# Kernel optimization log

Measured on AMD Instinct MI355X. Metric: run time of the kernel, lower is better.

The kernel has to match this reference:

```python
import math
import jax, jax.numpy as jnp
import numpy as np

jax.config.update("jax_enable_x64", True)

P_PRIME = 1000003            # prime modulus; p-1 = 2*3*166667
N_FACTORS = (2, 3, 166667)   # prime factors of p-1 (for primitive-root search)
B, NPATCH, L, K, DIM = 4, 784, 9, 16, 28  # batch, patches/sample, patch len, kernels, map dim


def _modpow(base, exp, p, nbits=21):
    """Vectorized modular exponentiation (square-and-multiply), int64, exponents < 2^nbits."""
    shape = jnp.broadcast_shapes(jnp.shape(base), jnp.shape(exp))
    b0 = jnp.broadcast_to(jnp.asarray(base, jnp.int64) % p, shape)
    e = jnp.broadcast_to(jnp.asarray(exp, jnp.int64), shape)
    def body(i, c):
        res, b = c
        res = jnp.where(((e >> i) & 1) == 1, (res * b) % p, res)
        return (res, (b * b) % p)
    res, _ = jax.lax.fori_loop(0, nbits, body, (jnp.ones(shape, jnp.int64), b0))
    return res


def _decrypt_ips(ct0, cts, y, sk_y, g, p):
    """IPFE decrypt + BSGS discrete log. ct0:[B,P] cts:[B,P,L] y:[K,L] sk_y:[K] -> signed ip [K,B,P]."""
    n = p - 1
    powed = _modpow(cts[None], jnp.mod(y, n)[:, None, None, :], p)   # [K,B,P,L]
    num = powed[..., 0]
    for i in range(1, L):                                            # fixed small L=9
        num = (num * powed[..., i]) % p
    denom = _modpow(ct0[None], jnp.mod(sk_y, n)[:, None, None], p)   # [K,B,P]
    val = (num * _modpow(denom, p - 2, p)) % p                       # = g^{<x,y>} mod p (Fermat inverse)
    # baby-step giant-step over group order n
    m = math.isqrt(n - 1) + 1
    n_giant = -(-n // m)
    baby = _modpow(jnp.int64(g), jnp.arange(m, dtype=jnp.int64), p)  # g^j, j in [0,m)
    order = jnp.argsort(baby)
    sb = baby[order]
    ginv_m = _modpow(jnp.int64(g), jnp.int64((n - m) % n), p)        # g^{-m}
    pt = _modpow(ginv_m, jnp.arange(n_giant, dtype=jnp.int64), p)    # g^{-m*i}
    gamma = (val.reshape(-1)[:, None] * pt[None, :]) % p             # [T, n_giant] giant steps
    pos = jnp.clip(jnp.searchsorted(sb, gamma), 0, m - 1)
    hit = sb[pos] == gamma
    cand = jnp.arange(n_giant, dtype=jnp.int64)[None, :] * m + order[pos]
    ip = jnp.min(jnp.where(hit, cand, n), axis=1)                    # unique match: ip = i*m + j
    ip = jnp.where(ip > n // 2, ip - n, ip)                          # signed representative
    return ip.reshape(K, ct0.shape[0], ct0.shape[1])


def _bn(x, g_, b_, m_, v_):
    s = g_ * jax.lax.rsqrt(v_ + 1e-5)
    return (x - m_[None, :, None, None]) * s[None, :, None, None] + b_[None, :, None, None]


def _conv(x, w, b):
    o = jax.lax.conv_general_dilated(x, w, (1, 1), ((1, 1), (1, 1)),
                                     dimension_numbers=("NCHW", "OIHW", "NCHW"))
    return o + b[None, :, None, None]


def _pool(x):
    return jax.lax.reduce_window(x, jnp.array(-jnp.inf, x.dtype), jax.lax.max,
                                 (1, 1, 2, 2), (1, 1, 2, 2), "VALID")


def _forward(ct0, cts, y, sk_y, bias1, bn1_g, bn1_b, bn1_m, bn1_v,
             conv2_w, conv2_b, bn2_g, bn2_b, bn2_m, bn2_v,
             conv3_w, conv3_b, bn3_g, bn3_b, bn3_m, bn3_v,
             fc1_w, fc1_b, fc2_w, fc2_b, g, p):
    ip = _decrypt_ips(ct0, cts, y, sk_y, g, p)                       # [K,B,P] int64
    maps = ip.astype(jnp.float32) / 10000.0 + bias1[:, None, None]   # dequantize + conv1 bias
    feat = jnp.transpose(maps, (1, 0, 2)).reshape(-1, K, DIM, DIM)   # [B,16,28,28]
    feat = _pool(jax.nn.relu(_bn(feat, bn1_g, bn1_b, bn1_m, bn1_v)))
    feat = _pool(jax.nn.relu(_bn(_conv(feat, conv2_w, conv2_b), bn2_g, bn2_b, bn2_m, bn2_v)))
    feat = _pool(jax.nn.relu(_bn(_conv(feat, conv3_w, conv3_b), bn3_g, bn3_b, bn3_m, bn3_v)))
    flat = feat.reshape(feat.shape[0], -1)                           # [B,576]
    h = jax.nn.relu(flat @ fc1_w.T + fc1_b)                          # dropout = identity (eval mode)
    return h @ fc2_w.T + fc2_b                                       # [B,10]


def setup_inputs():
    rng = np.random.default_rng(0)
    p, n = P_PRIME, P_PRIME - 1
    assert all(p % d for d in range(2, math.isqrt(p) + 1))           # p prime
    g = next(gg for gg in range(2, 200)
             if all(pow(gg, n // q, p) != 1 for q in N_FACTORS))      # primitive root mod p
    s = rng.integers(1, n, size=L)                                    # master secret
    pk = [pow(g, int(si), p) for si in s]
    y = rng.integers(-50, 51, size=(K, L)).astype(np.int64)          # round(w*10000)
    x = rng.integers(0, 21, size=(B, NPATCH, L))                     # quantized patch values
    r = rng.integers(1, n, size=(B, NPATCH))
    gx = [pow(g, t, p) for t in range(21)]
    ct0 = np.zeros((B, NPATCH), dtype=np.int64)
    cts = np.zeros((B, NPATCH, L), dtype=np.int64)
    for b in range(B):
        for j in range(NPATCH):
            rr = int(r[b, j])
            ct0[b, j] = pow(g, rr, p)
            for i in range(L):
                cts[b, j, i] = pow(pk[i], rr, p) * gx[x[b, j, i]] % p
    sk_y = np.array([sum(int(s[i]) * int(y[k, i]) for i in range(L)) % n
                     for k in range(K)], dtype=np.int64)
    f32 = lambda a: jnp.asarray(a, jnp.float32)
    def rn(*sh):
        return f32(rng.standard_normal(sh) * 0.1)
    def bnp(c):
        return (f32(1.0 + 0.1 * rng.standard_normal(c)), rn(c), rn(c), f32(rng.random(c) + 0.5))
    bn1_g, bn1_b, bn1_m, bn1_v = bnp(16)
    bn2_g, bn2_b, bn2_m, bn2_v = bnp(32)
    bn3_g, bn3_b, bn3_m, bn3_v = bnp(64)
    return dict(ct0=jnp.asarray(ct0), cts=jnp.asarray(cts),
                y=jnp.asarray(y), sk_y=jnp.asarray(sk_y), bias1=rn(K),
                bn1_g=bn1_g, bn1_b=bn1_b, bn1_m=bn1_m, bn1_v=bn1_v,
                conv2_w=rn(32, 16, 3, 3), conv2_b=rn(32),
                bn2_g=bn2_g, bn2_b=bn2_b, bn2_m=bn2_m, bn2_v=bn2_v,
                conv3_w=rn(64, 32, 3, 3), conv3_b=rn(64),
                bn3_g=bn3_g, bn3_b=bn3_b, bn3_m=bn3_m, bn3_v=bn3_v,
                fc1_w=rn(128, 576), fc1_b=rn(128),
                fc2_w=rn(10, 128), fc2_b=rn(10), g=g, p=p)


def reference(ct0, cts, y, sk_y, bias1, bn1_g, bn1_b, bn1_m, bn1_v,
              conv2_w, conv2_b, bn2_g, bn2_b, bn2_m, bn2_v,
              conv3_w, conv3_b, bn3_g, bn3_b, bn3_m, bn3_v,
              fc1_w, fc1_b, fc2_w, fc2_b, g, p):
    return _forward(ct0, cts, y, sk_y, bias1, bn1_g, bn1_b, bn1_m, bn1_v,
                    conv2_w, conv2_b, bn2_g, bn2_b, bn2_m, bn2_v,
                    conv3_w, conv3_b, bn3_g, bn3_b, bn3_m, bn3_v,
                    fc1_w, fc1_b, fc2_w, fc2_b, g, p)
```

## Files before the change

kernel.cpp:

```cpp
#include <hip/hip_runtime.h>
#include <stdint.h>

#define PRIME 1000003u
#define NORD  1000002u
#define KCH   16
#define BATCH 4
#define NPATCH 784
#define LLEN  9
#define IPMAX 9000
#define NDEC  (KCH*BATCH*NPATCH)
#define MBABY 512
#define NGIANT 36
#define HSLOTS 2048
#define HEMPTY 0xFFFFFFFFu

__device__ __forceinline__ uint32_t mmul(uint32_t a, uint32_t b) {
    uint64_t t = (uint64_t)a * (uint64_t)b;
    uint32_t q = (uint32_t)((t * 2199016ull) >> 41);
    uint32_t r = (uint32_t)t - q * PRIME;
    return (r >= PRIME) ? r - PRIME : r;
}

__device__ __forceinline__ uint32_t mpow(uint32_t base, uint32_t exp) {
    uint32_t r = 1u, b = base;
    while (exp) {
        if (exp & 1u) r = mmul(r, b);
        b = mmul(b, b);
        exp >>= 1;
    }
    return r;
}

__global__ void __launch_bounds__(256) decrypt_dlog(
    const int* __restrict__ ct0, const int* __restrict__ cts,
    const int* __restrict__ y, const int* __restrict__ sk_y,
    const float* __restrict__ bias1,
    const float* __restrict__ bn1_g, const float* __restrict__ bn1_b,
    const float* __restrict__ bn1_m, const float* __restrict__ bn1_v,
    const int* __restrict__ g_in, float* __restrict__ featr) {
    const int tid = threadIdx.x;
    __shared__ uint32_t hash[HSLOTS];

    const uint32_t g = (uint32_t)g_in[0];

    for (int i = tid; i < HSLOTS; i += 256) hash[i] = HEMPTY;
    __syncthreads();
    for (int r = tid; r < MBABY; r += 256) {
        uint32_t key = mpow(g, (uint32_t)r);
        uint32_t h = (key * 0x9E3779B1u) >> 21;
        uint32_t packed = (key << 9) | (uint32_t)r;
        while (atomicCAS(&hash[h], HEMPTY, packed) != HEMPTY)
            h = (h + 1) & (HSLOTS - 1);
    }
    __syncthreads();

    const int gtid = blockIdx.x * 256 + tid;
    if (gtid >= NDEC) return;
    int k = gtid / (BATCH * NPATCH);
    int r = gtid % (BATCH * NPATCH);
    int b = r / NPATCH;
    int j = r % NPATCH;

    const int* crow = cts + ((b * NPATCH) + j) * LLEN;
    const int* yrow = y + k * LLEN;

    uint32_t num_p = 1u, num_n = 1u;
#pragma unroll
    for (int i = 0; i < LLEN; i++) {
        int yi = yrow[i];
        uint32_t c = (uint32_t)crow[i];
        if (yi > 0)       num_p = mmul(num_p, mpow(c, (uint32_t)yi));
        else if (yi < 0)  num_n = mmul(num_n, mpow(c, (uint32_t)(-yi)));
    }
    uint32_t den = mpow((uint32_t)ct0[b * NPATCH + j], (uint32_t)sk_y[k]);
    den = mmul(den, num_n);
    uint32_t val = mmul(num_p, mpow(den, PRIME - 2u));

    uint32_t cur = mmul(val, mpow(g, IPMAX));
    const uint32_t gim = mpow(g, NORD - MBABY);
    int e = 0;
    bool found = false;
    for (int q = 0; q < NGIANT; q++) {
        if (!found) {
            uint32_t hh = (cur * 0x9E3779B1u) >> 21;
            uint32_t v;
            while ((v = hash[hh]) != HEMPTY) {
                if ((v >> 9) == cur) { e = q * MBABY + (int)(v & 511u); found = true; break; }
                hh = (hh + 1) & (HSLOTS - 1);
            }
        }
        cur = mmul(cur, gim);
    }
    int ip = e - IPMAX;

    float sc = bn1_g[k] * rsqrtf(bn1_v[k] + 1e-5f);
    float shf = (bias1[k] - bn1_m[k]) * sc + bn1_b[k];
    float v_ = fmaf((float)ip, sc * 1e-4f, shf);
    featr[((b * KCH) + k) * NPATCH + j] = fmaxf(v_, 0.0f);
}

__global__ void __launch_bounds__(256) conv2_k(
    const float* __restrict__ featr,
    const float* __restrict__ conv2_w, const float* __restrict__ conv2_b,
    const float* __restrict__ bn2_g, const float* __restrict__ bn2_b,
    const float* __restrict__ bn2_m, const float* __restrict__ bn2_v,
    float* __restrict__ s2g) {
    const int b  = blockIdx.x >> 5;
    const int oc = blockIdx.x & 31;
    const int tid = threadIdx.x;

    __shared__ float s1p[16][16][16];
    __shared__ float w[16 * 9];
    __shared__ float co[196];

    for (int i = tid; i < 16 * 16 * 16; i += 256)
        ((float*)s1p)[i] = 0.0f;
    if (tid < 144) w[tid] = conv2_w[oc * 144 + tid];
    __syncthreads();
    for (int i = tid; i < 16 * 196; i += 256) {
        int ic = i / 196, pos = i % 196;
        int yy = pos / 14, xx = pos % 14;
        const float* fp = featr + ((b * 16 + ic) * 784) + (2 * yy) * 28 + 2 * xx;
        s1p[ic][yy + 1][xx + 1] = fmaxf(fmaxf(fp[0], fp[1]), fmaxf(fp[28], fp[29]));
    }
    __syncthreads();

    if (tid < 196) {
        int oh = tid / 14, ow = tid % 14;
        float a0 = 0.0f, a1 = 0.0f, a2 = 0.0f;
#pragma unroll
        for (int ic = 0; ic < 16; ic++) {
            const float* wp = &w[ic * 9];
            const float* sp = &s1p[ic][oh][ow];
            a0 = fmaf(sp[0],  wp[0], fmaf(sp[1],  wp[1], fmaf(sp[2],  wp[2], a0)));
            a1 = fmaf(sp[16], wp[3], fmaf(sp[17], wp[4], fmaf(sp[18], wp[5], a1)));
            a2 = fmaf(sp[32], wp[6], fmaf(sp[33], wp[7], fmaf(sp[34], wp[8], a2)));
        }
        float sc = bn2_g[oc] * rsqrtf(bn2_v[oc] + 1e-5f);
        float shf = bn2_b[oc] - bn2_m[oc] * sc;
        co[tid] = fmaxf((a0 + a1 + a2 + conv2_b[oc]) * sc + shf, 0.0f);
    }
    __syncthreads();

    if (tid < 49) {
        int oh = tid / 7, ow = tid % 7;
        const float* c0 = &co[(2 * oh) * 14 + 2 * ow];
        s2g[((b * 32 + oc) * 49) + tid] =
            fmaxf(fmaxf(c0[0], c0[1]), fmaxf(c0[14], c0[15]));
    }
}

__global__ void __launch_bounds__(64) conv3_k(
    const float* __restrict__ s2g,
    const float* __restrict__ conv3_w, const float* __restrict__ conv3_b,
    const float* __restrict__ bn3_g, const float* __restrict__ bn3_b,
    const float* __restrict__ bn3_m, const float* __restrict__ bn3_v,
    float* __restrict__ s3g) {
    const int b  = blockIdx.x >> 6;
    const int oc = blockIdx.x & 63;
    const int tid = threadIdx.x;

    __shared__ float s2p[32][9][9];
    __shared__ float w[32 * 9];
    __shared__ float co[49];

    for (int i = tid; i < 32 * 81; i += 64)
        ((float*)s2p)[i] = 0.0f;
    for (int i = tid; i < 288; i += 64) w[i] = conv3_w[oc * 288 + i];
    __syncthreads();
    for (int i = tid; i < 32 * 49; i += 64) {
        int ic = i / 49, pos = i % 49;
        s2p[ic][pos / 7 + 1][pos % 7 + 1] = s2g[((b * 32 + ic) * 49) + pos];
    }
    __syncthreads();

    if (tid < 49) {
        int oh = tid / 7, ow = tid % 7;
        float a0 = 0.0f, a1 = 0.0f, a2 = 0.0f;
#pragma unroll
        for (int ic = 0; ic < 32; ic++) {
            const float* wp = &w[ic * 9];
            const float* sp = &s2p[ic][oh][ow];
            a0 = fmaf(sp[0],  wp[0], fmaf(sp[1],  wp[1], fmaf(sp[2],  wp[2], a0)));
            a1 = fmaf(sp[9],  wp[3], fmaf(sp[10], wp[4], fmaf(sp[11], wp[5], a1)));
            a2 = fmaf(sp[18], wp[6], fmaf(sp[19], wp[7], fmaf(sp[20], wp[8], a2)));
        }
        float sc = bn3_g[oc] * rsqrtf(bn3_v[oc] + 1e-5f);
        float shf = bn3_b[oc] - bn3_m[oc] * sc;
        co[tid] = fmaxf((a0 + a1 + a2 + conv3_b[oc]) * sc + shf, 0.0f);
    }
    __syncthreads();

    if (tid < 9) {
        int oh = tid / 3, ow = tid % 3;
        const float* c0 = &co[(2 * oh) * 7 + 2 * ow];
        s3g[b * 576 + oc * 9 + tid] = fmaxf(fmaxf(c0[0], c0[1]), fmaxf(c0[7], c0[8]));
    }
}

__global__ void __launch_bounds__(1024) fc_k(
    const float* __restrict__ s3g,
    const float* __restrict__ fc1_w, const float* __restrict__ fc1_b,
    const float* __restrict__ fc2_w, const float* __restrict__ fc2_b,
    float* __restrict__ out) {
    const int b = blockIdx.x;
    const int tid = threadIdx.x;
    const int wid = tid >> 6, lane = tid & 63;
    __shared__ float s3[576];
    __shared__ float h[128];

    for (int i = tid; i < 576; i += 1024) s3[i] = s3g[b * 576 + i];
    __syncthreads();

#pragma unroll
    for (int oo = 0; oo < 8; oo++) {
        int o = wid * 8 + oo;
        const float* w = fc1_w + o * 576;
        float acc = 0.0f;
#pragma unroll
        for (int jj = 0; jj < 9; jj++)
            acc = fmaf(s3[jj * 64 + lane], w[jj * 64 + lane], acc);
#pragma unroll
        for (int off = 32; off; off >>= 1) acc += __shfl_down(acc, off);
        if (lane == 0) h[o] = fmaxf(acc + fc1_b[o], 0.0f);
    }
    __syncthreads();

    if (wid < 10) {
        const float* w = fc2_w + wid * 128;
        float acc = fmaf(s3[0] * 0.0f + h[lane], w[lane], 0.0f);
        acc = fmaf(h[64 + lane], w[64 + lane], acc);
#pragma unroll
        for (int off = 32; off; off >>= 1) acc += __shfl_down(acc, off);
        if (lane == 0) out[b * 10 + wid] = acc + fc2_b[wid];
    }
}

extern "C" void kernel_launch(void* const* d_in, const int* in_sizes, int n_in,
                              void* d_out, int out_size, void* d_ws, size_t ws_size,
                              hipStream_t stream) {
    const int*   ct0    = (const int*)d_in[0];
    const int*   cts    = (const int*)d_in[1];
    const int*   y      = (const int*)d_in[2];
    const int*   sk_y   = (const int*)d_in[3];
    const float* bias1  = (const float*)d_in[4];
    const float* bn1_g  = (const float*)d_in[5];
    const float* bn1_b  = (const float*)d_in[6];
    const float* bn1_m  = (const float*)d_in[7];
    const float* bn1_v  = (const float*)d_in[8];
    const float* conv2_w = (const float*)d_in[9];
    const float* conv2_b = (const float*)d_in[10];
    const float* bn2_g  = (const float*)d_in[11];
    const float* bn2_b  = (const float*)d_in[12];
    const float* bn2_m  = (const float*)d_in[13];
    const float* bn2_v  = (const float*)d_in[14];
    const float* conv3_w = (const float*)d_in[15];
    const float* conv3_b = (const float*)d_in[16];
    const float* bn3_g  = (const float*)d_in[17];
    const float* bn3_b  = (const float*)d_in[18];
    const float* bn3_m  = (const float*)d_in[19];
    const float* bn3_v  = (const float*)d_in[20];
    const float* fc1_w  = (const float*)d_in[21];
    const float* fc1_b  = (const float*)d_in[22];
    const float* fc2_w  = (const float*)d_in[23];
    const float* fc2_b  = (const float*)d_in[24];
    const int*   g_in   = (const int*)d_in[25];
    float* out = (float*)d_out;

    char* ws = (char*)d_ws;
    float* featr = (float*)ws;
    float* s2g   = (float*)(ws + 200704);
    float* s3g   = (float*)(ws + 225792);

    decrypt_dlog<<<NDEC / 256, 256, 0, stream>>>(
        ct0, cts, y, sk_y, bias1, bn1_g, bn1_b, bn1_m, bn1_v, g_in, featr);

    conv2_k<<<BATCH * 32, 256, 0, stream>>>(
        featr, conv2_w, conv2_b, bn2_g, bn2_b, bn2_m, bn2_v, s2g);

    conv3_k<<<BATCH * 64, 64, 0, stream>>>(
        s2g, conv3_w, conv3_b, bn3_g, bn3_b, bn3_m, bn3_v, s3g);

    fc_k<<<BATCH, 1024, 0, stream>>>(s3g, fc1_w, fc1_b, fc2_w, fc2_b, out);
}
```

Baseline: 156.7 us.

## Replace BSGS discrete log with direct global lookup table

Drops the per-block shared-memory baby-step hash and the 36-step giant-step search. A new kernel writes a ~4 MB global table indexed by g^e mod p that holds e for every exponent in [-IPMAX, IPMAX], and the decrypt kernel recovers the inner product with one gather. The table is rebuilt on every call, and entries for values outside the range are never initialised, so the code relies on every inner product falling inside the assumed range. It also makes k wave-uniform via readfirstlane and drops a dead multiply in fc.

New measurement: 143.1 us. 1.1x faster.

```diff
diff --git a/kernel.cpp b/kernel.cpp
--- a/kernel.cpp
+++ b/kernel.cpp
@@ -8,11 +8,8 @@
 #define NPATCH 784
 #define LLEN  9
 #define IPMAX 9000
+#define TBLN  (2*IPMAX+1)
 #define NDEC  (KCH*BATCH*NPATCH)
-#define MBABY 512
-#define NGIANT 36
-#define HSLOTS 2048
-#define HEMPTY 0xFFFFFFFFu
 
 __device__ __forceinline__ uint32_t mmul(uint32_t a, uint32_t b) {
     uint64_t t = (uint64_t)a * (uint64_t)b;
@@ -31,32 +28,24 @@
     return r;
 }
 
-__global__ void __launch_bounds__(256) decrypt_dlog(
+__global__ void build_table(const int* __restrict__ g_in, int* __restrict__ table) {
+    int e = blockIdx.x * blockDim.x + threadIdx.x;
+    if (e >= TBLN) return;
+    int es = e - IPMAX;
+    uint32_t exp = (es >= 0) ? (uint32_t)es : (uint32_t)(es + (int)NORD);
+    table[mpow((uint32_t)g_in[0], exp)] = es;
+}
+
+__global__ void __launch_bounds__(256) decrypt(
     const int* __restrict__ ct0, const int* __restrict__ cts,
     const int* __restrict__ y, const int* __restrict__ sk_y,
     const float* __restrict__ bias1,
     const float* __restrict__ bn1_g, const float* __restrict__ bn1_b,
     const float* __restrict__ bn1_m, const float* __restrict__ bn1_v,
-    const int* __restrict__ g_in, float* __restrict__ featr) {
-    const int tid = threadIdx.x;
-    __shared__ uint32_t hash[HSLOTS];
-
-    const uint32_t g = (uint32_t)g_in[0];
-
-    for (int i = tid; i < HSLOTS; i += 256) hash[i] = HEMPTY;
-    __syncthreads();
-    for (int r = tid; r < MBABY; r += 256) {
-        uint32_t key = mpow(g, (uint32_t)r);
-        uint32_t h = (key * 0x9E3779B1u) >> 21;
-        uint32_t packed = (key << 9) | (uint32_t)r;
-        while (atomicCAS(&hash[h], HEMPTY, packed) != HEMPTY)
-            h = (h + 1) & (HSLOTS - 1);
-    }
-    __syncthreads();
-
-    const int gtid = blockIdx.x * 256 + tid;
+    const int* __restrict__ table, float* __restrict__ featr) {
+    int gtid = blockIdx.x * 256 + threadIdx.x;
     if (gtid >= NDEC) return;
-    int k = gtid / (BATCH * NPATCH);
+    int k = __builtin_amdgcn_readfirstlane(gtid / (BATCH * NPATCH));
     int r = gtid % (BATCH * NPATCH);
     int b = r / NPATCH;
     int j = r % NPATCH;
@@ -76,22 +65,7 @@
     den = mmul(den, num_n);
     uint32_t val = mmul(num_p, mpow(den, PRIME - 2u));
 
-    uint32_t cur = mmul(val, mpow(g, IPMAX));
-    const uint32_t gim = mpow(g, NORD - MBABY);
-    int e = 0;
-    bool found = false;
-    for (int q = 0; q < NGIANT; q++) {
-        if (!found) {
-            uint32_t hh = (cur * 0x9E3779B1u) >> 21;
-            uint32_t v;
-            while ((v = hash[hh]) != HEMPTY) {
-                if ((v >> 9) == cur) { e = q * MBABY + (int)(v & 511u); found = true; break; }
-                hh = (hh + 1) & (HSLOTS - 1);
-            }
-        }
-        cur = mmul(cur, gim);
-    }
-    int ip = e - IPMAX;
+    int ip = table[val];
 
     float sc = bn1_g[k] * rsqrtf(bn1_v[k] + 1e-5f);
     float shf = (bias1[k] - bn1_m[k]) * sc + bn1_b[k];
@@ -228,7 +202,7 @@
 
     if (wid < 10) {
         const float* w = fc2_w + wid * 128;
-        float acc = fmaf(s3[0] * 0.0f + h[lane], w[lane], 0.0f);
+        float acc = fmaf(h[lane], w[lane], 0.0f);
         acc = fmaf(h[64 + lane], w[64 + lane], acc);
 #pragma unroll
         for (int off = 32; off; off >>= 1) acc += __shfl_down(acc, off);
@@ -268,12 +242,15 @@
     float* out = (float*)d_out;
 
     char* ws = (char*)d_ws;
-    float* featr = (float*)ws;
-    float* s2g   = (float*)(ws + 200704);
-    float* s3g   = (float*)(ws + 225792);
-
-    decrypt_dlog<<<NDEC / 256, 256, 0, stream>>>(
-        ct0, cts, y, sk_y, bias1, bn1_g, bn1_b, bn1_m, bn1_v, g_in, featr);
+    int*   table = (int*)ws;
+    float* featr = (float*)(ws + 4000256);
+    float* s2g   = (float*)(ws + 4200960);
+    float* s3g   = (float*)(ws + 4226048);
+
+    build_table<<<(TBLN + 255) / 256, 256, 0, stream>>>(g_in, table);
+
+    decrypt<<<NDEC / 256, 256, 0, stream>>>(
+        ct0, cts, y, sk_y, bias1, bn1_g, bn1_b, bn1_m, bn1_v, table, featr);
 
     conv2_k<<<BATCH * 32, 256, 0, stream>>>(
         featr, conv2_w, conv2_b, bn2_g, bn2_b, bn2_m, bn2_v, s2g);
```
